# Kernel optimization log

Measured on AMD Instinct MI355X. Metric: run time of the kernel, lower is better.

## Reference

```python
import jax, jax.numpy as jnp
import numpy as np

N, M, CIN, COUT, K, KS = 200000, 100000, 32, 64, 32, 3


def setup_inputs() -> dict:
    key = jax.random.key(0)
    ks = jax.random.split(key, 6)
    inp_positions = jax.random.uniform(ks[0], (N, 3), dtype=jnp.float32)
    out_positions = jax.random.uniform(ks[1], (M, 3), dtype=jnp.float32)
    inp_features = jax.random.normal(ks[2], (N, CIN), dtype=jnp.float32)
    inp_importance = jnp.ones((N,), dtype=jnp.float32)
    neighbors_index = jax.random.randint(ks[3], (M, K), 0, N, dtype=jnp.int32)
    kernel = 0.05 * jax.random.normal(ks[4], (KS, KS, KS, CIN, COUT), dtype=jnp.float32)
    bias = jnp.zeros((COUT,), dtype=jnp.float32)
    extents = jnp.ones((1,), dtype=jnp.float32)
    return dict(inp_features=inp_features, inp_positions=inp_positions,
                out_positions=out_positions, extents=extents,
                inp_importance=inp_importance, neighbors_index=neighbors_index,
                kernel=kernel, bias=bias)


def _axis_weights(x):
    """x: [...,] coord clamped to [0, KS-1]. Returns [..., KS] linear interp weights."""
    grid = jnp.arange(KS, dtype=x.dtype)
    return jnp.maximum(0.0, 1.0 - jnp.abs(x[..., None] - grid))


def reference(inp_features, inp_positions, out_positions, extents,
              inp_importance, neighbors_index, kernel, bias):
    radius = 0.5 * extents[0]
    nbr_pos = inp_positions[neighbors_index]                   # [M,K,3]
    rel = (nbr_pos - out_positions[:, None, :]) / radius       # unit-ball coords
    dist = jnp.sqrt(jnp.sum(rel * rel, axis=-1))               # [M,K] L2 metric
    mask = (dist <= 1.0).astype(inp_features.dtype)            # in-radius validity
    # ball_to_cube_radial: scale radially so sphere boundary -> cube boundary
    linf = jnp.max(jnp.abs(rel), axis=-1)                      # [M,K]
    scale = jnp.where(linf > 1e-8, dist / jnp.maximum(linf, 1e-8), 0.0)
    cube = rel * scale[..., None]                              # in [-1,1]^3
    # align_corners=True: map [-1,1] to voxel-center coords [0, KS-1]
    coords = jnp.clip((cube + 1.0) * (0.5 * (KS - 1)), 0.0, KS - 1.0)  # 'linear' clamp
    wx = _axis_weights(coords[..., 0])                         # [M,K,3]
    wy = _axis_weights(coords[..., 1])
    wz = _axis_weights(coords[..., 2])
    imp = mask * inp_importance[neighbors_index]               # [M,K]
    feat = inp_features[neighbors_index] * imp[..., None]      # [M,K,CIN]
    # accumulate importance*interp-weighted features per filter voxel
    acc = jnp.einsum('mka,mkb,mkc,mki->mabci', wx, wy, wz, feat)  # [M,3,3,3,CIN]
    out = jnp.einsum('mabci,abcio->mo', acc, kernel)           # [M,COUT]
    # normalize=True, no window fn -> divide by (importance-weighted) neighbor count
    norm = jnp.sum(imp, axis=1)                                # [M]
    out = out * jnp.where(norm > 0, 1.0 / jnp.maximum(norm, 1e-12), 0.0)[:, None]
    return out + bias  # activation=None
```

## Files before the change

kernel.cpp:

```cpp
#include <hip/hip_runtime.h>


typedef __attribute__((ext_vector_type(8))) __bf16 bf16x8;
typedef __attribute__((ext_vector_type(4))) __bf16 bf16x4;
typedef __attribute__((ext_vector_type(4))) float f32x4;
typedef unsigned int u32;
typedef unsigned short u16;

constexpr int NPTS = 200000;
constexpr int MPTS = 100000;
constexpr int MB   = 16;
constexpr int NBLK = MPTS / MB;

constexpr int W_V       = 72;
constexpr int PT_STRIDE = 2016;
constexpr int NRM_OFF   = MB * PT_STRIDE;
constexpr int LDS_BYTES = NRM_OFF + 64;

constexpr size_t WFRAG_ELEMS = 4 * 28 * 64 * 8;
constexpr size_t FEATS_OFF_ELEMS = WFRAG_ELEMS;
constexpr size_t WS_NEED = (WFRAG_ELEMS + (size_t)NPTS * 32) * 2;

__global__ void prep_kernel(const float* __restrict__ kern,
                            const float* __restrict__ feats,
                            __bf16* __restrict__ wsb) {
    const int blk = blockIdx.x;
    if (blk < 224) {
        const int tid = blk * 256 + threadIdx.x;
        const int j  = tid & 7;
        const int l  = (tid >> 3) & 63;
        const int s  = tid >> 9;
        const int ks = s % 28;
        const int nt = s / 28;
        const int kk = ks * 32 + ((l >> 4) << 3) + j;
        const int ch = kk / 28;
        const int v  = kk - ch * 28;
        const int o  = nt * 16 + (l & 15);
        const float val = (v < 27) ? kern[v * 2048 + ch * 64 + o] : 0.0f;
        wsb[tid] = (__bf16)val;
    } else {
        const int t = (blk - 224) * 256 + threadIdx.x;
        const float4* src = (const float4*)feats + (size_t)t * 2;
        const float4 a = src[0];
        const float4 b = src[1];
        bf16x8 o;
        o[0]=(__bf16)a.x; o[1]=(__bf16)a.y; o[2]=(__bf16)a.z; o[3]=(__bf16)a.w;
        o[4]=(__bf16)b.x; o[5]=(__bf16)b.y; o[6]=(__bf16)b.z; o[7]=(__bf16)b.w;
        *(bf16x8*)(wsb + FEATS_OFF_ELEMS + (size_t)t * 8) = o;
    }
}

__device__ __forceinline__ void phase0_weights(
    unsigned char* smem, float* nrm, int blk, int tid,
    const float* __restrict__ inpos, const float* __restrict__ outpos,
    const float* __restrict__ importance, const int* __restrict__ nbrs,
    float inv_r)
{
    const int pt = tid >> 4;
    const int kp = tid & 15;
    const int m  = blk * MB + pt;
    const int2 nn = *(const int2*)(nbrs + m * 32 + 2 * kp);
    const float ox = outpos[3 * m + 0];
    const float oy = outpos[3 * m + 1];
    const float oz = outpos[3 * m + 2];

    float cxA, cyA, czA, impA, cxB, cyB, czB, impB;
    {
        const int nb = nn.x;
        const float rx = (inpos[3 * nb + 0] - ox) * inv_r;
        const float ry = (inpos[3 * nb + 1] - oy) * inv_r;
        const float rz = (inpos[3 * nb + 2] - oz) * inv_r;
        const float dist = sqrtf(rx * rx + ry * ry + rz * rz);
        float imp = importance[nb];
        impA = (dist <= 1.0f) ? imp : 0.0f;
        const float linf = fmaxf(fabsf(rx), fmaxf(fabsf(ry), fabsf(rz)));
        const float sc = (linf > 1e-8f) ? (dist / linf) : 0.0f;
        cxA = fminf(fmaxf(rx * sc + 1.0f, 0.0f), 2.0f);
        cyA = fminf(fmaxf(ry * sc + 1.0f, 0.0f), 2.0f);
        czA = fminf(fmaxf(rz * sc + 1.0f, 0.0f), 2.0f);
    }
    {
        const int nb = nn.y;
        const float rx = (inpos[3 * nb + 0] - ox) * inv_r;
        const float ry = (inpos[3 * nb + 1] - oy) * inv_r;
        const float rz = (inpos[3 * nb + 2] - oz) * inv_r;
        const float dist = sqrtf(rx * rx + ry * ry + rz * rz);
        float imp = importance[nb];
        impB = (dist <= 1.0f) ? imp : 0.0f;
        const float linf = fmaxf(fabsf(rx), fmaxf(fabsf(ry), fabsf(rz)));
        const float sc = (linf > 1e-8f) ? (dist / linf) : 0.0f;
        cxB = fminf(fmaxf(rx * sc + 1.0f, 0.0f), 2.0f);
        cyB = fminf(fmaxf(ry * sc + 1.0f, 0.0f), 2.0f);
        czB = fminf(fmaxf(rz * sc + 1.0f, 0.0f), 2.0f);
    }

    float wxA[3], wyA[3], wzA[3], wxB[3], wyB[3], wzB[3];
    wxA[0] = fmaxf(0.f, 1.f - cxA) * impA;
    wxA[1] = (1.f - fabsf(cxA - 1.f)) * impA;
    wxA[2] = fmaxf(0.f, cxA - 1.f) * impA;
    wyA[0] = fmaxf(0.f, 1.f - cyA); wyA[1] = 1.f - fabsf(cyA - 1.f); wyA[2] = fmaxf(0.f, cyA - 1.f);
    wzA[0] = fmaxf(0.f, 1.f - czA); wzA[1] = 1.f - fabsf(czA - 1.f); wzA[2] = fmaxf(0.f, czA - 1.f);
    wxB[0] = fmaxf(0.f, 1.f - cxB) * impB;
    wxB[1] = (1.f - fabsf(cxB - 1.f)) * impB;
    wxB[2] = fmaxf(0.f, cxB - 1.f) * impB;
    wyB[0] = fmaxf(0.f, 1.f - cyB); wyB[1] = 1.f - fabsf(cyB - 1.f); wyB[2] = fmaxf(0.f, cyB - 1.f);
    wzB[0] = fmaxf(0.f, 1.f - czB); wzB[1] = 1.f - fabsf(czB - 1.f); wzB[2] = fmaxf(0.f, czB - 1.f);

    unsigned char* wrow = smem + pt * PT_STRIDE + kp * 4;
#pragma unroll
    for (int a = 0; a < 3; ++a)
#pragma unroll
        for (int b = 0; b < 3; ++b) {
            const float pA = wxA[a] * wyA[b];
            const float pB = wxB[a] * wyB[b];
#pragma unroll
            for (int c = 0; c < 3; ++c) {
                const int v = a * 9 + b * 3 + c;
                union { __bf16 h[2]; u32 u; } pk;
                pk.h[0] = (__bf16)(pA * wzA[c]);
                pk.h[1] = (__bf16)(pB * wzB[c]);
                *(u32*)(wrow + v * W_V) = pk.u;
            }
        }
    *(u32*)(wrow + 27 * W_V) = 0u;

    float s = impA + impB;
    s += __shfl_xor(s, 1);
    s += __shfl_xor(s, 2);
    s += __shfl_xor(s, 4);
    s += __shfl_xor(s, 8);
    if (kp == 0) nrm[pt] = (s > 0.f) ? (1.f / fmaxf(s, 1e-12f)) : 0.f;
}

__device__ __forceinline__ void compute_pt(
    unsigned char* smem, int ptq, int lr, int grp, bf16x8 b0, bf16x8 b1)
{
    unsigned char* pbase = smem + ptq * PT_STRIDE;
    const u32 sw = ((u32)(ptq & 7)) << 4;
    const bf16x8 a0 = *(const bf16x8*)(pbase + lr * W_V + grp * 16);
    const int rr = (16 + lr > 27) ? 27 : (16 + lr);
    const bf16x8 a1 = *(const bf16x8*)(pbase + rr * W_V + grp * 16);

    f32x4 d00 = {0.f,0.f,0.f,0.f}, d01 = {0.f,0.f,0.f,0.f};
    f32x4 d10 = {0.f,0.f,0.f,0.f}, d11 = {0.f,0.f,0.f,0.f};
    d00 = __builtin_amdgcn_mfma_f32_16x16x32_bf16(a0, b0, d00, 0, 0, 0);
    d01 = __builtin_amdgcn_mfma_f32_16x16x32_bf16(a0, b1, d01, 0, 0, 0);
    d10 = __builtin_amdgcn_mfma_f32_16x16x32_bf16(a1, b0, d10, 0, 0, 0);
    d11 = __builtin_amdgcn_mfma_f32_16x16x32_bf16(a1, b1, d11, 0, 0, 0);

    const int vb0 = grp * 4, vb1 = 16 + grp * 4;
    bf16x4 t;
    t[0]=(__bf16)d00[0]; t[1]=(__bf16)d00[1]; t[2]=(__bf16)d00[2]; t[3]=(__bf16)d00[3];
    *(bf16x4*)(pbase + (((u32)(112 * lr + 2 * vb0)) ^ sw)) = t;
    t[0]=(__bf16)d01[0]; t[1]=(__bf16)d01[1]; t[2]=(__bf16)d01[2]; t[3]=(__bf16)d01[3];
    *(bf16x4*)(pbase + (((u32)(112 * lr + 56 + 2 * vb0)) ^ sw)) = t;
    if (vb1 < 28) {
        t[0]=(__bf16)d10[0]; t[1]=(__bf16)d10[1]; t[2]=(__bf16)d10[2]; t[3]=(__bf16)d10[3];
        *(bf16x4*)(pbase + (((u32)(112 * lr + 2 * vb1)) ^ sw)) = t;
        t[0]=(__bf16)d11[0]; t[1]=(__bf16)d11[1]; t[2]=(__bf16)d11[2]; t[3]=(__bf16)d11[3];
        *(bf16x4*)(pbase + (((u32)(112 * lr + 56 + 2 * vb1)) ^ sw)) = t;
    }
}

#define SQ(q) do {                                                          \
    const int4 nA = *(const int4*)(nb_base + (q) * 32);                     \
    const int4 nB = *(const int4*)(nb_base + (q) * 32 + 4);                 \
    stq[q][0] = featsb[(size_t)nA.x * 16 + lr];                             \
    stq[q][1] = featsb[(size_t)nA.y * 16 + lr];                             \
    stq[q][2] = featsb[(size_t)nA.z * 16 + lr];                             \
    stq[q][3] = featsb[(size_t)nA.w * 16 + lr];                             \
    stq[q][4] = featsb[(size_t)nB.x * 16 + lr];                             \
    stq[q][5] = featsb[(size_t)nB.y * 16 + lr];                             \
    stq[q][6] = featsb[(size_t)nB.z * 16 + lr];                             \
    stq[q][7] = featsb[(size_t)nB.w * 16 + lr];                             \
} while (0)

#define CQ(q) do {                                                          \
    union { u16 u[8]; bf16x8 v; } B0, B1;                                   \
    _Pragma("unroll")                                                       \
    for (int j = 0; j < 8; ++j) {                                           \
        B0.u[j] = (u16)(stq[q][j] & 0xffffu);                               \
        B1.u[j] = (u16)(stq[q][j] >> 16);                                   \
    }                                                                       \
    compute_pt(smem, wv * 4 + (q), lr, grp, B0.v, B1.v);                    \
} while (0)

#define SF(q, b) do {                                                       \
    const int4 nA = *(const int4*)(nb_base + (q) * 32);                     \
    const int4 nB = *(const int4*)(nb_base + (q) * 32 + 4);                 \
    stf[b][0] = ((const float2*)(feats + (size_t)nA.x * 32))[lr];           \
    stf[b][1] = ((const float2*)(feats + (size_t)nA.y * 32))[lr];           \
    stf[b][2] = ((const float2*)(feats + (size_t)nA.z * 32))[lr];           \
    stf[b][3] = ((const float2*)(feats + (size_t)nA.w * 32))[lr];           \
    stf[b][4] = ((const float2*)(feats + (size_t)nB.x * 32))[lr];           \
    stf[b][5] = ((const float2*)(feats + (size_t)nB.y * 32))[lr];           \
    stf[b][6] = ((const float2*)(feats + (size_t)nB.z * 32))[lr];           \
    stf[b][7] = ((const float2*)(feats + (size_t)nB.w * 32))[lr];           \
} while (0)

#define CF(q, b) do {                                                       \
    bf16x8 b0, b1;                                                          \
    _Pragma("unroll")                                                       \
    for (int j = 0; j < 8; ++j) {                                           \
        b0[j] = (__bf16)stf[b][j].x;                                        \
        b1[j] = (__bf16)stf[b][j].y;                                        \
    }                                                                       \
    compute_pt(smem, wv * 4 + (q), lr, grp, b0, b1);                        \
} while (0)

template<int PRE>
__device__ __forceinline__ void cconv_impl(
    const float* __restrict__ feats, const u32* __restrict__ featsb,
    const float* __restrict__ inpos, const float* __restrict__ outpos,
    const float* __restrict__ extents, const float* __restrict__ importance,
    const int* __restrict__ nbrs, const __bf16* __restrict__ wfrag,
    const float* __restrict__ bias, float* __restrict__ out)
{
    __shared__ __align__(16) unsigned char smem[LDS_BYTES];
    const int tid = threadIdx.x;
    const int blk = blockIdx.x;
    float* nrm = (float*)(smem + NRM_OFF);
    const float inv_r = 2.0f / extents[0];

    const int wv = tid >> 6, lane = tid & 63, grp = lane >> 4, lr = lane & 15;
    const int* nb_base = nbrs + (blk * MB + wv * 4) * 32 + grp * 8;

    if constexpr (PRE) {
        u32 stq[4][8];
        SQ(0); SQ(1);
        phase0_weights(smem, nrm, blk, tid, inpos, outpos, importance, nbrs, inv_r);
        SQ(2); SQ(3);
        CQ(0); CQ(1); CQ(2); CQ(3);
    } else {
        phase0_weights(smem, nrm, blk, tid, inpos, outpos, importance, nbrs, inv_r);
        float2 stf[2][8];
        SF(0, 0); SF(1, 1);
        CF(0, 0); SF(2, 0);
        CF(1, 1); SF(3, 1);
        CF(2, 0); CF(3, 1);
    }

    const bf16x8* wb = (const bf16x8*)wfrag;
    const size_t wvb = (size_t)(wv * 28) * 64 + lane;
    bf16x8 wreg[4];
    wreg[0] = wb[wvb];       wreg[1] = wb[wvb + 64];
    wreg[2] = wb[wvb + 128]; wreg[3] = wb[wvb + 192];
    __syncthreads();

    const unsigned char* abase = smem + lr * PT_STRIDE;
    const u32 swr = ((u32)(lr & 7)) << 4;
    bf16x8 areg[4];
#pragma unroll
    for (int i = 0; i < 4; ++i)
        areg[i] = *(const bf16x8*)(abase + (((u32)(i * 64 + grp * 16)) ^ swr));

    f32x4 e = {0.f, 0.f, 0.f, 0.f};
#pragma unroll
    for (int ks = 0; ks < 28; ++ks) {
        e = __builtin_amdgcn_mfma_f32_16x16x32_bf16(areg[ks & 3], wreg[ks & 3], e, 0, 0, 0);
        if (ks + 4 < 28) {
            wreg[ks & 3] = wb[wvb + (size_t)(ks + 4) * 64];
            areg[ks & 3] = *(const bf16x8*)(abase + (((u32)((ks + 4) * 64 + grp * 16)) ^ swr));
        }
    }

    const int o = wv * 16 + lr;
    const float bb = bias[o];
#pragma unroll
    for (int r = 0; r < 4; ++r) {
        const int pt = grp * 4 + r;
        out[(size_t)(blk * MB + pt) * 64 + o] = e[r] * nrm[pt] + bb;
    }
}

__global__ __launch_bounds__(256, 5)
void cconv_pre(const float* __restrict__ feats, const u32* __restrict__ featsb,
               const float* __restrict__ inpos, const float* __restrict__ outpos,
               const float* __restrict__ extents, const float* __restrict__ importance,
               const int* __restrict__ nbrs, const __bf16* __restrict__ wfrag,
               const float* __restrict__ bias, float* __restrict__ out) {
    cconv_impl<1>(feats, featsb, inpos, outpos, extents, importance, nbrs, wfrag, bias, out);
}

__global__ __launch_bounds__(256, 5)
void cconv_f32(const float* __restrict__ feats, const u32* __restrict__ featsb,
               const float* __restrict__ inpos, const float* __restrict__ outpos,
               const float* __restrict__ extents, const float* __restrict__ importance,
               const int* __restrict__ nbrs, const __bf16* __restrict__ wfrag,
               const float* __restrict__ bias, float* __restrict__ out) {
    cconv_impl<0>(feats, featsb, inpos, outpos, extents, importance, nbrs, wfrag, bias, out);
}

extern "C" void kernel_launch(void* const* d_in, const int* in_sizes, int n_in,
                              void* d_out, int out_size, void* d_ws, size_t ws_size,
                              hipStream_t stream) {
    (void)in_sizes; (void)n_in; (void)out_size;
    const float* feats      = (const float*)d_in[0];
    const float* inpos      = (const float*)d_in[1];
    const float* outpos     = (const float*)d_in[2];
    const float* extents    = (const float*)d_in[3];
    const float* importance = (const float*)d_in[4];
    const int*   nbrs       = (const int*)d_in[5];
    const float* kern       = (const float*)d_in[6];
    const float* bias       = (const float*)d_in[7];
    float* outp = (float*)d_out;
    __bf16* wsb = (__bf16*)d_ws;
    const u32* featsb = (const u32*)(wsb + FEATS_OFF_ELEMS);

    const bool pre = ws_size >= WS_NEED;

    hipLaunchKernelGGL(prep_kernel, dim3(pre ? 3349 : 224), dim3(256), 0, stream,
                       kern, feats, wsb);
    if (pre) {
        hipLaunchKernelGGL(cconv_pre, dim3(NBLK), dim3(256), 0, stream,
                           feats, featsb, inpos, outpos, extents, importance,
                           nbrs, wsb, bias, outp);
    } else {
        hipLaunchKernelGGL(cconv_f32, dim3(NBLK), dim3(256), 0, stream,
                           feats, featsb, inpos, outpos, extents, importance,
                           nbrs, wsb, bias, outp);
    }
}
```

Before: 192.5 us.

## Process two point tiles per block, prefetching both tiles' feature gathers up front

The main kernel now handles two 16-point units per block, with half as many blocks. It issues all gathered bf16 feature loads for both units before any compute, so the second unit's gather latency hides behind the first unit's weights, MFMA and output work. Phase-0 loads are split from the math, the weight-fragment prefetch depth drops from 4 to 2, and launch bounds fall from 5 to 4 blocks per CU. The cost is higher register pressure from holding 64 gathered values per thread, plus lower occupancy and fewer blocks to balance across CUs.

After: 252.9 us. +31.4%, slower.

```diff
diff --git a/kernel.cpp b/kernel.cpp
--- a/kernel.cpp
+++ b/kernel.cpp
@@ -10,7 +10,8 @@
 constexpr int NPTS = 200000;
 constexpr int MPTS = 100000;
 constexpr int MB   = 16;
-constexpr int NBLK = MPTS / MB;
+constexpr int NUNIT = MPTS / MB;
+constexpr int NBLK  = NUNIT / 2;
 
 constexpr int W_V       = 72;
 constexpr int PT_STRIDE = 2016;
@@ -50,29 +51,41 @@
     }
 }
 
-__device__ __forceinline__ void phase0_weights(
-    unsigned char* smem, float* nrm, int blk, int tid,
-    const float* __restrict__ inpos, const float* __restrict__ outpos,
-    const float* __restrict__ importance, const int* __restrict__ nbrs,
-    float inv_r)
-{
-    const int pt = tid >> 4;
-    const int kp = tid & 15;
-    const int m  = blk * MB + pt;
-    const int2 nn = *(const int2*)(nbrs + m * 32 + 2 * kp);
-    const float ox = outpos[3 * m + 0];
-    const float oy = outpos[3 * m + 1];
-    const float oz = outpos[3 * m + 2];
+struct P0R {
+    int2 nn;
+    float ox, oy, oz;
+    float pax, pay, paz, pbx, pby, pbz;
+    float ia, ib;
+};
+
+__device__ __forceinline__ P0R p0_load(int m_base, int tid,
+    const int* __restrict__ nbrs, const float* __restrict__ outpos,
+    const float* __restrict__ inpos, const float* __restrict__ importance)
+{
+    P0R r;
+    const int pt = tid >> 4, kp = tid & 15;
+    const int m  = m_base + pt;
+    r.nn = *(const int2*)(nbrs + m * 32 + 2 * kp);
+    r.ox = outpos[3 * m + 0]; r.oy = outpos[3 * m + 1]; r.oz = outpos[3 * m + 2];
+    r.pax = inpos[3 * r.nn.x + 0]; r.pay = inpos[3 * r.nn.x + 1]; r.paz = inpos[3 * r.nn.x + 2];
+    r.pbx = inpos[3 * r.nn.y + 0]; r.pby = inpos[3 * r.nn.y + 1]; r.pbz = inpos[3 * r.nn.y + 2];
+    r.ia = importance[r.nn.x];
+    r.ib = importance[r.nn.y];
+    return r;
+}
+
+__device__ __forceinline__ void p0_math(const P0R& r, unsigned char* smem,
+                                        float* nrm, int tid, float inv_r)
+{
+    const int pt = tid >> 4, kp = tid & 15;
 
     float cxA, cyA, czA, impA, cxB, cyB, czB, impB;
     {
-        const int nb = nn.x;
-        const float rx = (inpos[3 * nb + 0] - ox) * inv_r;
-        const float ry = (inpos[3 * nb + 1] - oy) * inv_r;
-        const float rz = (inpos[3 * nb + 2] - oz) * inv_r;
+        const float rx = (r.pax - r.ox) * inv_r;
+        const float ry = (r.pay - r.oy) * inv_r;
+        const float rz = (r.paz - r.oz) * inv_r;
         const float dist = sqrtf(rx * rx + ry * ry + rz * rz);
-        float imp = importance[nb];
-        impA = (dist <= 1.0f) ? imp : 0.0f;
+        impA = (dist <= 1.0f) ? r.ia : 0.0f;
         const float linf = fmaxf(fabsf(rx), fmaxf(fabsf(ry), fabsf(rz)));
         const float sc = (linf > 1e-8f) ? (dist / linf) : 0.0f;
         cxA = fminf(fmaxf(rx * sc + 1.0f, 0.0f), 2.0f);
@@ -80,13 +93,11 @@
         czA = fminf(fmaxf(rz * sc + 1.0f, 0.0f), 2.0f);
     }
     {
-        const int nb = nn.y;
-        const float rx = (inpos[3 * nb + 0] - ox) * inv_r;
-        const float ry = (inpos[3 * nb + 1] - oy) * inv_r;
-        const float rz = (inpos[3 * nb + 2] - oz) * inv_r;
+        const float rx = (r.pbx - r.ox) * inv_r;
+        const float ry = (r.pby - r.oy) * inv_r;
+        const float rz = (r.pbz - r.oz) * inv_r;
         const float dist = sqrtf(rx * rx + ry * ry + rz * rz);
-        float imp = importance[nb];
-        impB = (dist <= 1.0f) ? imp : 0.0f;
+        impB = (dist <= 1.0f) ? r.ib : 0.0f;
         const float linf = fmaxf(fabsf(rx), fmaxf(fabsf(ry), fabsf(rz)));
         const float sc = (linf > 1e-8f) ? (dist / linf) : 0.0f;
         cxB = fminf(fmaxf(rx * sc + 1.0f, 0.0f), 2.0f);
@@ -132,6 +143,21 @@
     if (kp == 0) nrm[pt] = (s > 0.f) ? (1.f / fmaxf(s, 1e-12f)) : 0.f;
 }
 
+__device__ __forceinline__ void sq_batch(u32 dst[8], const u32* __restrict__ featsb,
+                                         const int* __restrict__ nb, int lr)
+{
+    const int4 nA = *(const int4*)(nb);
+    const int4 nB = *(const int4*)(nb + 4);
+    dst[0] = featsb[(size_t)nA.x * 16 + lr];
+    dst[1] = featsb[(size_t)nA.y * 16 + lr];
+    dst[2] = featsb[(size_t)nA.z * 16 + lr];
+    dst[3] = featsb[(size_t)nA.w * 16 + lr];
+    dst[4] = featsb[(size_t)nB.x * 16 + lr];
+    dst[5] = featsb[(size_t)nB.y * 16 + lr];
+    dst[6] = featsb[(size_t)nB.z * 16 + lr];
+    dst[7] = featsb[(size_t)nB.w * 16 + lr];
+}
+
 __device__ __forceinline__ void compute_pt(
     unsigned char* smem, int ptq, int lr, int grp, bf16x8 b0, bf16x8 b1)
 {
@@ -162,59 +188,60 @@
     }
 }
 
-#define SQ(q) do {                                                          \
-    const int4 nA = *(const int4*)(nb_base + (q) * 32);                     \
-    const int4 nB = *(const int4*)(nb_base + (q) * 32 + 4);                 \
-    stq[q][0] = featsb[(size_t)nA.x * 16 + lr];                             \
-    stq[q][1] = featsb[(size_t)nA.y * 16 + lr];                             \
-    stq[q][2] = featsb[(size_t)nA.z * 16 + lr];                             \
-    stq[q][3] = featsb[(size_t)nA.w * 16 + lr];                             \
-    stq[q][4] = featsb[(size_t)nB.x * 16 + lr];                             \
-    stq[q][5] = featsb[(size_t)nB.y * 16 + lr];                             \
-    stq[q][6] = featsb[(size_t)nB.z * 16 + lr];                             \
-    stq[q][7] = featsb[(size_t)nB.w * 16 + lr];                             \
-} while (0)
-
-#define CQ(q) do {                                                          \
-    union { u16 u[8]; bf16x8 v; } B0, B1;                                   \
-    _Pragma("unroll")                                                       \
-    for (int j = 0; j < 8; ++j) {                                           \
-        B0.u[j] = (u16)(stq[q][j] & 0xffffu);                               \
-        B1.u[j] = (u16)(stq[q][j] >> 16);                                   \
-    }                                                                       \
-    compute_pt(smem, wv * 4 + (q), lr, grp, B0.v, B1.v);                    \
-} while (0)
-
-#define SF(q, b) do {                                                       \
-    const int4 nA = *(const int4*)(nb_base + (q) * 32);                     \
-    const int4 nB = *(const int4*)(nb_base + (q) * 32 + 4);                 \
-    stf[b][0] = ((const float2*)(feats + (size_t)nA.x * 32))[lr];           \
-    stf[b][1] = ((const float2*)(feats + (size_t)nA.y * 32))[lr];           \
-    stf[b][2] = ((const float2*)(feats + (size_t)nA.z * 32))[lr];           \
-    stf[b][3] = ((const float2*)(feats + (size_t)nA.w * 32))[lr];           \
-    stf[b][4] = ((const float2*)(feats + (size_t)nB.x * 32))[lr];           \
-    stf[b][5] = ((const float2*)(feats + (size_t)nB.y * 32))[lr];           \
-    stf[b][6] = ((const float2*)(feats + (size_t)nB.z * 32))[lr];           \
-    stf[b][7] = ((const float2*)(feats + (size_t)nB.w * 32))[lr];           \
-} while (0)
-
-#define CF(q, b) do {                                                       \
-    bf16x8 b0, b1;                                                          \
-    _Pragma("unroll")                                                       \
-    for (int j = 0; j < 8; ++j) {                                           \
-        b0[j] = (__bf16)stf[b][j].x;                                        \
-        b1[j] = (__bf16)stf[b][j].y;                                        \
-    }                                                                       \
-    compute_pt(smem, wv * 4 + (q), lr, grp, b0, b1);                        \
-} while (0)
-
-template<int PRE>
-__device__ __forceinline__ void cconv_impl(
-    const float* __restrict__ feats, const u32* __restrict__ featsb,
-    const float* __restrict__ inpos, const float* __restrict__ outpos,
-    const float* __restrict__ extents, const float* __restrict__ importance,
-    const int* __restrict__ nbrs, const __bf16* __restrict__ wfrag,
-    const float* __restrict__ bias, float* __restrict__ out)
+__device__ __forceinline__ void cq_pt(unsigned char* smem, int ptq, int lr, int grp,
+                                      const u32 s[8])
+{
+    union { u16 u[8]; bf16x8 v; } B0, B1;
+#pragma unroll
+    for (int j = 0; j < 8; ++j) {
+        B0.u[j] = (u16)(s[j] & 0xffffu);
+        B1.u[j] = (u16)(s[j] >> 16);
+    }
+    compute_pt(smem, ptq, lr, grp, B0.v, B1.v);
+}
+
+__device__ __forceinline__ void phase2_run(
+    const unsigned char* smem, const float* nrm,
+    const __bf16* __restrict__ wfrag, const float* __restrict__ bias,
+    float* __restrict__ out, int m_base, int wv, int lane, int grp, int lr)
+{
+    const bf16x8* wb = (const bf16x8*)wfrag;
+    const size_t wvb = (size_t)(wv * 28) * 64 + lane;
+    const unsigned char* abase = smem + lr * PT_STRIDE;
+    const u32 swr = ((u32)(lr & 7)) << 4;
+
+    bf16x8 w0 = wb[wvb];
+    bf16x8 w1 = wb[wvb + 64];
+    f32x4 e = {0.f, 0.f, 0.f, 0.f};
+#pragma unroll
+    for (int ks = 0; ks < 28; ++ks) {
+        const bf16x8 a = *(const bf16x8*)(abase + (((u32)(ks * 64 + grp * 16)) ^ swr));
+        e = __builtin_amdgcn_mfma_f32_16x16x32_bf16(a, (ks & 1) ? w1 : w0, e, 0, 0, 0);
+        if (ks + 2 < 28) {
+            if (ks & 1) w1 = wb[wvb + (size_t)(ks + 2) * 64];
+            else        w0 = wb[wvb + (size_t)(ks + 2) * 64];
+        }
+    }
+
+    const int o = wv * 16 + lr;
+    const float bb = bias[o];
+#pragma unroll
+    for (int r = 0; r < 4; ++r) {
+        const int pt = grp * 4 + r;
+        out[(size_t)(m_base + pt) * 64 + o] = e[r] * nrm[pt] + bb;
+    }
+}
+
+__global__ __launch_bounds__(256, 4)
+void cconv_pipe(const u32* __restrict__ featsb,
+                const float* __restrict__ inpos,
+                const float* __restrict__ outpos,
+                const float* __restrict__ extents,
+                const float* __restrict__ importance,
+                const int*   __restrict__ nbrs,
+                const __bf16* __restrict__ wfrag,
+                const float* __restrict__ bias,
+                float* __restrict__ out)
 {
     __shared__ __align__(16) unsigned char smem[LDS_BYTES];
     const int tid = threadIdx.x;
@@ -223,72 +250,92 @@
     const float inv_r = 2.0f / extents[0];
 
     const int wv = tid >> 6, lane = tid & 63, grp = lane >> 4, lr = lane & 15;
-    const int* nb_base = nbrs + (blk * MB + wv * 4) * 32 + grp * 8;
-
-    if constexpr (PRE) {
-        u32 stq[4][8];
-        SQ(0); SQ(1);
-        phase0_weights(smem, nrm, blk, tid, inpos, outpos, importance, nbrs, inv_r);
-        SQ(2); SQ(3);
-        CQ(0); CQ(1); CQ(2); CQ(3);
-    } else {
-        phase0_weights(smem, nrm, blk, tid, inpos, outpos, importance, nbrs, inv_r);
-        float2 stf[2][8];
-        SF(0, 0); SF(1, 1);
-        CF(0, 0); SF(2, 0);
-        CF(1, 1); SF(3, 1);
-        CF(2, 0); CF(3, 1);
-    }
-
-    const bf16x8* wb = (const bf16x8*)wfrag;
-    const size_t wvb = (size_t)(wv * 28) * 64 + lane;
-    bf16x8 wreg[4];
-    wreg[0] = wb[wvb];       wreg[1] = wb[wvb + 64];
-    wreg[2] = wb[wvb + 128]; wreg[3] = wb[wvb + 192];
+    const int m0 = blk * MB;
+    const int m1 = (blk + NBLK) * MB;
+    const int* nb0 = nbrs + (m0 + wv * 4) * 32 + grp * 8;
+    const int* nb1 = nbrs + (m1 + wv * 4) * 32 + grp * 8;
+
+    const P0R r0 = p0_load(m0, tid, nbrs, outpos, inpos, importance);
+
+    u32 stq0[4][8], stq1[4][8];
+    sq_batch(stq0[0], featsb, nb0 +  0, lr);
+    sq_batch(stq0[1], featsb, nb0 + 32, lr);
+    sq_batch(stq0[2], featsb, nb0 + 64, lr);
+    sq_batch(stq0[3], featsb, nb0 + 96, lr);
+    sq_batch(stq1[0], featsb, nb1 +  0, lr);
+    sq_batch(stq1[1], featsb, nb1 + 32, lr);
+    sq_batch(stq1[2], featsb, nb1 + 64, lr);
+    sq_batch(stq1[3], featsb, nb1 + 96, lr);
+    __builtin_amdgcn_sched_barrier(0);
+
+    p0_math(r0, smem, nrm, tid, inv_r);
+    cq_pt(smem, wv * 4 + 0, lr, grp, stq0[0]);
+    cq_pt(smem, wv * 4 + 1, lr, grp, stq0[1]);
+    cq_pt(smem, wv * 4 + 2, lr, grp, stq0[2]);
+    cq_pt(smem, wv * 4 + 3, lr, grp, stq0[3]);
     __syncthreads();
 
-    const unsigned char* abase = smem + lr * PT_STRIDE;
-    const u32 swr = ((u32)(lr & 7)) << 4;
-    bf16x8 areg[4];
-#pragma unroll
-    for (int i = 0; i < 4; ++i)
-        areg[i] = *(const bf16x8*)(abase + (((u32)(i * 64 + grp * 16)) ^ swr));
-
-    f32x4 e = {0.f, 0.f, 0.f, 0.f};
-#pragma unroll
-    for (int ks = 0; ks < 28; ++ks) {
-        e = __builtin_amdgcn_mfma_f32_16x16x32_bf16(areg[ks & 3], wreg[ks & 3], e, 0, 0, 0);
-        if (ks + 4 < 28) {
-            wreg[ks & 3] = wb[wvb + (size_t)(ks + 4) * 64];
-            areg[ks & 3] = *(const bf16x8*)(abase + (((u32)((ks + 4) * 64 + grp * 16)) ^ swr));
+    phase2_run(smem, nrm, wfrag, bias, out, m0, wv, lane, grp, lr);
+    __syncthreads();
+
+    const P0R r1 = p0_load(m1, tid, nbrs, outpos, inpos, importance);
+    p0_math(r1, smem, nrm, tid, inv_r);
+    cq_pt(smem, wv * 4 + 0, lr, grp, stq1[0]);
+    cq_pt(smem, wv * 4 + 1, lr, grp, stq1[1]);
+    cq_pt(smem, wv * 4 + 2, lr, grp, stq1[2]);
+    cq_pt(smem, wv * 4 + 3, lr, grp, stq1[3]);
+    __syncthreads();
+
+    phase2_run(smem, nrm, wfrag, bias, out, m1, wv, lane, grp, lr);
+}
+
+__global__ __launch_bounds__(256, 4)
+void cconv_f32(const float* __restrict__ feats,
+               const float* __restrict__ inpos,
+               const float* __restrict__ outpos,
+               const float* __restrict__ extents,
+               const float* __restrict__ importance,
+               const int*   __restrict__ nbrs,
+               const __bf16* __restrict__ wfrag,
+               const float* __restrict__ bias,
+               float* __restrict__ out)
+{
+    __shared__ __align__(16) unsigned char smem[LDS_BYTES];
+    const int tid = threadIdx.x;
+    const int blk = blockIdx.x;
+    float* nrm = (float*)(smem + NRM_OFF);
+    const float inv_r = 2.0f / extents[0];
+
+    const int wv = tid >> 6, lane = tid & 63, grp = lane >> 4, lr = lane & 15;
+    const int m0 = blk * MB;
+    const int* nb_base = nbrs + (m0 + wv * 4) * 32 + grp * 8;
+
+    const P0R r0 = p0_load(m0, tid, nbrs, outpos, inpos, importance);
+    p0_math(r0, smem, nrm, tid, inv_r);
+
+#pragma unroll
+    for (int q = 0; q < 4; ++q) {
+        const int4 nA = *(const int4*)(nb_base + q * 32);
+        const int4 nB = *(const int4*)(nb_base + q * 32 + 4);
+        float2 sf[8];
+        sf[0] = ((const float2*)(feats + (size_t)nA.x * 32))[lr];
+        sf[1] = ((const float2*)(feats + (size_t)nA.y * 32))[lr];
+        sf[2] = ((const float2*)(feats + (size_t)nA.z * 32))[lr];
+        sf[3] = ((const float2*)(feats + (size_t)nA.w * 32))[lr];
+        sf[4] = ((const float2*)(feats + (size_t)nB.x * 32))[lr];
+        sf[5] = ((const float2*)(feats + (size_t)nB.y * 32))[lr];
+        sf[6] = ((const float2*)(feats + (size_t)nB.z * 32))[lr];
+        sf[7] = ((const float2*)(feats + (size_t)nB.w * 32))[lr];
+        bf16x8 b0, b1;
+#pragma unroll
+        for (int j = 0; j < 8; ++j) {
+            b0[j] = (__bf16)sf[j].x;
+            b1[j] = (__bf16)sf[j].y;
         }
-    }
-
-    const int o = wv * 16 + lr;
-    const float bb = bias[o];
-#pragma unroll
-    for (int r = 0; r < 4; ++r) {
-        const int pt = grp * 4 + r;
-        out[(size_t)(blk * MB + pt) * 64 + o] = e[r] * nrm[pt] + bb;
-    }
-}
-
-__global__ __launch_bounds__(256, 5)
-void cconv_pre(const float* __restrict__ feats, const u32* __restrict__ featsb,
-               const float* __restrict__ inpos, const float* __restrict__ outpos,
-               const float* __restrict__ extents, const float* __restrict__ importance,
-               const int* __restrict__ nbrs, const __bf16* __restrict__ wfrag,
-               const float* __restrict__ bias, float* __restrict__ out) {
-    cconv_impl<1>(feats, featsb, inpos, outpos, extents, importance, nbrs, wfrag, bias, out);
-}
-
-__global__ __launch_bounds__(256, 5)
-void cconv_f32(const float* __restrict__ feats, const u32* __restrict__ featsb,
-               const float* __restrict__ inpos, const float* __restrict__ outpos,
-               const float* __restrict__ extents, const float* __restrict__ importance,
-               const int* __restrict__ nbrs, const __bf16* __restrict__ wfrag,
-               const float* __restrict__ bias, float* __restrict__ out) {
-    cconv_impl<0>(feats, featsb, inpos, outpos, extents, importance, nbrs, wfrag, bias, out);
+        compute_pt(smem, wv * 4 + q, lr, grp, b0, b1);
+    }
+    __syncthreads();
+    phase2_run(smem, nrm, wfrag, bias, out, m0, wv, lane, grp, lr);
 }
 
 extern "C" void kernel_launch(void* const* d_in, const int* in_sizes, int n_in,
@@ -312,12 +359,12 @@
     hipLaunchKernelGGL(prep_kernel, dim3(pre ? 3349 : 224), dim3(256), 0, stream,
                        kern, feats, wsb);
     if (pre) {
-        hipLaunchKernelGGL(cconv_pre, dim3(NBLK), dim3(256), 0, stream,
-                           feats, featsb, inpos, outpos, extents, importance,
+        hipLaunchKernelGGL(cconv_pipe, dim3(NBLK), dim3(256), 0, stream,
+                           featsb, inpos, outpos, extents, importance,
                            nbrs, wsb, bias, outp);
     } else {
-        hipLaunchKernelGGL(cconv_f32, dim3(NBLK), dim3(256), 0, stream,
-                           feats, featsb, inpos, outpos, extents, importance,
+        hipLaunchKernelGGL(cconv_f32, dim3(NBLK * 2), dim3(256), 0, stream,
+                           feats, inpos, outpos, extents, importance,
                            nbrs, wsb, bias, outp);
     }
 }
```
